# Kernel optimization log

Measured on AMD Instinct MI355X. Metric: run time of the kernel, lower is better.

## Reference

```python
import jax, jax.numpy as jnp
import numpy as np

N, S, EMB, H = 8, 1024, 512, 8
D = EMB // H  # head_dim = 64


def setup_inputs() -> dict:
    key = jax.random.key(0)
    ks = jax.random.split(key, 12)
    f = lambda k_, shp, s=1.0: jax.random.normal(k_, shp, dtype=jnp.float32) * s
    return {
        "v": f(ks[0], (N, S, EMB)),
        "k": f(ks[1], (N, S, EMB)),
        "q": f(ks[2], (N, S, EMB)),
        "Wv": f(ks[3], (D, D), 0.02), "bv": jnp.zeros((D,), jnp.float32),
        "Wk": f(ks[4], (D, D), 0.02), "bk": jnp.zeros((D,), jnp.float32),
        "Wq": f(ks[5], (D, D), 0.02), "bq": jnp.zeros((D,), jnp.float32),
        "E": f(ks[6], (1, S, D), 0.02),   # relative-position embedding
        "Wo": f(ks[7], (EMB, EMB), 0.02), "bo": jnp.zeros((EMB,), jnp.float32),
    }


def reference(v, k, q, Wv, bv, Wk, bk, Wq, bq, E, Wo, bo):
    n = v.shape[0]
    # per-head linear projections (module == 'spatiotemporal' branch)
    vals = v.reshape(n, S, H, D) @ Wv.T + bv   # (n,S,H,D)
    keys = k.reshape(n, S, H, D) @ Wk.T + bk
    qrs = q.reshape(n, S, H, D) @ Wq.T + bq

    # relative-position bias via skew trick (uses VALUES, as in source)
    QE = jnp.einsum('nlhd,sd->nhls', vals, E[0])            # (n,H,S,S)
    flip_mask = jnp.flip(jnp.triu(jnp.ones((S, S), bool), 1), axis=1)
    QE = jnp.where(flip_mask, 0.0, QE)                      # _mask_positions
    padded = jnp.pad(QE, ((0, 0), (0, 0), (0, 0), (1, 0)))  # left-pad last dim
    Sbias = padded.reshape(n, H, S + 1, S)[:, :, 1:, :]     # _skew -> (n,H,S,S)

    # attention scores with the source's mask semantics:
    # masked_fill(mask == 0, -1e20) keeps entries where triu(...,1) == 1
    qk = jnp.einsum('nqhd,nkhd->nhqk', qrs, keys)           # (n,H,S,S)
    keep = jnp.triu(jnp.ones((S, S), bool), 1)
    qk = jnp.where(keep, qk, jnp.float32(-1e20))

    attn = jax.nn.softmax(qk / jnp.sqrt(jnp.float32(EMB)), axis=3) + Sbias

    z = jnp.einsum('nhql,nlhd->nqhd', attn, vals).reshape(n, S, EMB)
    return z @ Wo.T + bo
```

## Files before the change

### kernel.cpp

```cpp
#include <hip/hip_runtime.h>
#include <hip/hip_bf16.h>

#define SDIM 1024
#define HNUM 8
#define DDIM 64
#define EMBD 512
#define NBATCH 8

static constexpr float SCALE = 0.044194173824159216f;

typedef short bf16x8 __attribute__((ext_vector_type(8)));
typedef float f32x4 __attribute__((ext_vector_type(4)));

__device__ __forceinline__ ushort bf16_of(float f) {
    return __builtin_bit_cast(unsigned short, __float2bfloat16(f));
}
__device__ __forceinline__ float f32_of(ushort u) {
    return __bfloat162float(__builtin_bit_cast(__hip_bfloat16, u));
}

__device__ __forceinline__ bf16x8 lds8(const ushort* base, int row, int slot) {
    return *(const bf16x8*)(base + (row * 8 + (slot ^ (row & 7))) * 8);
}

#define MFMA(a, b, c) __builtin_amdgcn_mfma_f32_16x16x32_bf16(a, b, c, 0, 0, 0)

__global__ __launch_bounds__(256) void proj_mfma(
    const float* __restrict__ xv, const float* __restrict__ xk, const float* __restrict__ xq,
    const float* __restrict__ Wv, const float* __restrict__ bv,
    const float* __restrict__ Wk, const float* __restrict__ bk,
    const float* __restrict__ Wq, const float* __restrict__ bq,
    ushort* __restrict__ vals_bf, ushort* __restrict__ keys_bf, ushort* __restrict__ qrs_bf)
{
    __shared__ ushort a_s[256 * 64];
    __shared__ ushort w_s[64 * 64];

    const int blk = blockIdx.x;
    const int m = blk % 3;
    const int chunk = blk / 3;
    const int tok0 = chunk * 32;
    const int n = tok0 >> 10, s0 = tok0 & 1023;
    const int t = threadIdx.x;
    const int w = t >> 6, l = t & 63, lrow = l & 15, lgrp = l >> 4;

    const float* X = (m == 0) ? xv : (m == 1) ? xk : xq;
    const float* W = (m == 0) ? Wv : (m == 1) ? Wk : Wq;
    const float* B = (m == 0) ? bv : (m == 1) ? bk : bq;
    ushort* O = (m == 0) ? vals_bf : (m == 1) ? keys_bf : qrs_bf;

    #pragma unroll
    for (int i = 0; i < 16; ++i) {
        const int f4 = i * 256 + t;
        const int ls = f4 >> 7, c4 = f4 & 127;
        const int h = c4 >> 4, d4 = c4 & 15;
        const float4 v = ((const float4*)(X + (size_t)(tok0 + ls) * EMBD))[c4];
        ushort4 u;
        u.x = bf16_of(v.x); u.y = bf16_of(v.y); u.z = bf16_of(v.z); u.w = bf16_of(v.w);
        const int r = h * 32 + ls, slot = d4 >> 1;
        *(ushort4*)(a_s + (r * 8 + (slot ^ (r & 7))) * 8 + (d4 & 1) * 4) = u;
    }
    #pragma unroll
    for (int i = 0; i < 4; ++i) {
        const int f4 = i * 256 + t;
        const int r = f4 >> 4, d4 = f4 & 15;
        const float4 v = ((const float4*)W)[f4];
        ushort4 u;
        u.x = bf16_of(v.x); u.y = bf16_of(v.y); u.z = bf16_of(v.z); u.w = bf16_of(v.w);
        const int slot = d4 >> 1;
        *(ushort4*)(w_s + (r * 8 + (slot ^ (r & 7))) * 8 + (d4 & 1) * 4) = u;
    }
    __syncthreads();

    f32x4 acc[4][4];
    #pragma unroll
    for (int fr = 0; fr < 4; ++fr)
        #pragma unroll
        for (int fc = 0; fc < 4; ++fc) acc[fr][fc] = {0.f, 0.f, 0.f, 0.f};

    bf16x8 af[4][2];
    #pragma unroll
    for (int fr = 0; fr < 4; ++fr)
        #pragma unroll
        for (int kc = 0; kc < 2; ++kc)
            af[fr][kc] = lds8(a_s, w * 64 + fr * 16 + lrow, lgrp + kc * 4);

    #pragma unroll
    for (int fc = 0; fc < 4; ++fc)
        #pragma unroll
        for (int kc = 0; kc < 2; ++kc) {
            const bf16x8 bfr = lds8(w_s, fc * 16 + lrow, lgrp + kc * 4);
            #pragma unroll
            for (int fr = 0; fr < 4; ++fr)
                acc[fr][fc] = MFMA(af[fr][kc], bfr, acc[fr][fc]);
        }
    __syncthreads();

    float bias[4];
    #pragma unroll
    for (int fc = 0; fc < 4; ++fc) bias[fc] = B[fc * 16 + lrow];
    #pragma unroll
    for (int fr = 0; fr < 4; ++fr)
        #pragma unroll
        for (int fc = 0; fc < 4; ++fc)
            #pragma unroll
            for (int reg = 0; reg < 4; ++reg) {
                const int row = w * 64 + fr * 16 + lgrp * 4 + reg;
                const int col = fc * 16 + lrow;
                a_s[(row * 8 + ((col >> 3) ^ (row & 7))) * 8 + (col & 7)] =
                    bf16_of(acc[fr][fc][reg] + bias[fc]);
            }
    __syncthreads();

    #pragma unroll
    for (int i = 0; i < 8; ++i) {
        const int cc = i * 256 + t;
        const int r = cc >> 3, slot = cc & 7;
        const int h = r >> 5, ls = r & 31;
        const float4 v = *(const float4*)(a_s + (r * 8 + (slot ^ (r & 7))) * 8);
        *(float4*)(O + ((size_t)(n * HNUM + h) * SDIM + s0 + ls) * DDIM + slot * 8) = v;
    }
}

__global__ __launch_bounds__(256) void conv_e(const float* __restrict__ E, ushort* __restrict__ e_bf) {
    const int i = blockIdx.x * 256 + threadIdx.x;
    e_bf[i] = bf16_of(E[i]);
}
__global__ __launch_bounds__(256) void conv_wo(const float* __restrict__ Wo, ushort* __restrict__ wo_bf) {
    const int i = blockIdx.x * 256 + threadIdx.x;
    wo_bf[i] = bf16_of(Wo[i]);
}

__global__ __launch_bounds__(256) void transpose_vals(
    const ushort* __restrict__ vals_bf, ushort* __restrict__ valsT_bf)
{
    __shared__ ushort tile[64][72];
    const int blk = blockIdx.x;
    const int st = blk & 15, nh = blk >> 4;
    const int s0 = st * 64;
    const int t = threadIdx.x;
    const ushort* src = vals_bf + (nh * SDIM + s0) * DDIM;
    #pragma unroll
    for (int i = 0; i < 2; ++i) {
        const int c = t + i * 256;
        const int row = c >> 3, slot = c & 7;
        const float4 vv = ((const float4*)src)[c];
        *(float4*)&tile[row][slot * 8] = vv;
    }
    __syncthreads();
    const int d = t >> 2, si = (t & 3) * 16;
    union { ushort u[16]; float4 f[2]; } buf;
    #pragma unroll
    for (int u2 = 0; u2 < 16; ++u2) buf.u[u2] = tile[si + u2][d];
    float4* dst = (float4*)(valsT_bf + (nh * DDIM + d) * SDIM + s0 + si);
    dst[0] = buf.f[0];
    dst[1] = buf.f[1];
}

__global__ __launch_bounds__(512, 2) void attn_mfma(
    const ushort* __restrict__ vals_bf, const ushort* __restrict__ keys_bf,
    const ushort* __restrict__ qrs_bf, const ushort* __restrict__ valsT_bf,
    const ushort* __restrict__ e_bf, ushort* __restrict__ zh)
{
    __shared__ ushort k_s [64 * 64];
    __shared__ ushort vt_s[64 * 64];
    __shared__ ushort e_s [192 * 64];
    __shared__ ushort pe_s[128 * 64];
    __shared__ ushort pb_s[128 * 64];
    __shared__ float  vs_s[64];

    const int vid = blockIdx.x;
    const int blk = (vid & 7) * 64 + (vid >> 3);
    const int bt = blk & 7, h = (blk >> 3) & 7, n = blk >> 6;
    const int i0 = bt * 128;
    const int t = threadIdx.x;
    const int w = t >> 6, l = t & 63, lrow = l & 15, lgrp = l >> 4;
    const int s = w >> 2, q = w & 3;
    const int myit = 2 * bt + s;
    const int eoff = (1 - s) * 64;

    const ushort* Qb  = qrs_bf   + (n * HNUM + h) * (SDIM * DDIM);
    const ushort* Kb  = keys_bf  + (n * HNUM + h) * (SDIM * DDIM);
    const ushort* Vb  = vals_bf  + (n * HNUM + h) * (SDIM * DDIM);
    const ushort* VTb = valsT_bf + (n * HNUM + h) * (SDIM * DDIM);

    bf16x8 a_q[2], a_vi[2];
    {
        const int grow = i0 + w * 16 + lrow;
        #pragma unroll
        for (int kc = 0; kc < 2; ++kc) {
            a_q[kc]  = *(const bf16x8*)(Qb + grow * DDIM + kc * 32 + lgrp * 8);
            a_vi[kc] = *(const bf16x8*)(Vb + grow * DDIM + kc * 32 + lgrp * 8);
        }
    }
    if (t < 64) vs_s[t] = 0.f;

    f32x4 accn[4], accz[4];
    #pragma unroll
    for (int f = 0; f < 4; ++f) {
        accn[f] = {0.f, 0.f, 0.f, 0.f};
        accz[f] = {0.f, 0.f, 0.f, 0.f};
    }
    float den[4] = {0.f, 0.f, 0.f, 0.f};

    for (int jt = 0; jt < 16; ++jt) {
        const int j0 = jt * 64;
        const bool diag = (jt == myit);
        const bool needK = (jt >= 2 * bt);
        const bool needE = (jt <= 2 * bt + 1);
        __syncthreads();

        {
            const int row = t >> 3, slot = t & 7;
            const int sw = (row * 8 + (slot ^ (row & 7))) * 8;
            *(float4*)(vt_s + sw) = *(const float4*)(VTb + row * SDIM + j0 + slot * 8);
            if (needK)
                *(float4*)(k_s + sw) = *(const float4*)(Kb + (j0 + row) * DDIM + slot * 8);
        }
        if (needE) {
            const int ebU = SDIM - 128 - i0 + j0;
            #pragma unroll
            for (int i = 0; i < 3; ++i) {
                const int c = t + i * 512;
                const int row = c >> 3, slot = c & 7;
                const int g = ebU + row;
                float4 vv = make_float4(0.f, 0.f, 0.f, 0.f);
                if (g < SDIM) vv = *(const float4*)(e_bf + g * DDIM + slot * 8);
                *(float4*)(e_s + (row * 8 + (slot ^ (row & 7))) * 8) = vv;
            }
        }
        __syncthreads();

        if (bt == 7 && t < 64) {
            float sum = 0.f;
            #pragma unroll
            for (int slot = 0; slot < 8; ++slot) {
                const bf16x8 vv = lds8(vt_s, t, slot);
                #pragma unroll
                for (int u = 0; u < 8; ++u) sum += f32_of((ushort)vv[u]);
            }
            vs_s[t] += sum;
        }

        if (jt >= myit) {
            f32x4 sf[4];
            #pragma unroll
            for (int fc = 0; fc < 4; ++fc) sf[fc] = {0.f, 0.f, 0.f, 0.f};
            #pragma unroll
            for (int fc = 0; fc < 4; ++fc)
                if (!diag || fc >= q)
                    #pragma unroll
                    for (int kc = 0; kc < 2; ++kc)
                        sf[fc] = MFMA(a_q[kc], lds8(k_s, fc * 16 + lrow, lgrp + kc * 4), sf[fc]);
            #pragma unroll
            for (int fc = 0; fc < 4; ++fc) {
                #pragma unroll
                for (int r = 0; r < 4; ++r) {
                    const int rs = q * 16 + lgrp * 4 + r;
                    const int col = fc * 16 + lrow;
                    float e = 0.f;
                    if (!diag || col > rs) e = __expf(sf[fc][r] * SCALE);
                    den[r] += e;
                    const int prow = w * 16 + lgrp * 4 + r;
                    pe_s[(prow * 8 + ((col >> 3) ^ (prow & 7))) * 8 + (col & 7)] = bf16_of(e);
                }
            }
            bf16x8 ap[2];
            #pragma unroll
            for (int kc = 0; kc < 2; ++kc) ap[kc] = lds8(pe_s, w * 16 + lrow, lgrp + kc * 4);
            #pragma unroll
            for (int fc = 0; fc < 4; ++fc)
                #pragma unroll
                for (int kc = 0; kc < 2; ++kc)
                    accn[fc] = MFMA(ap[kc], lds8(vt_s, fc * 16 + lrow, lgrp + kc * 4), accn[fc]);
        }

        if (jt <= myit) {
            #pragma unroll
            for (int half = 0; half < 2; ++half) {
                f32x4 bd[4];
                #pragma unroll
                for (int fq = 0; fq < 4; ++fq) bd[fq] = {0.f, 0.f, 0.f, 0.f};
                #pragma unroll
                for (int fq = 0; fq < 4; ++fq) {
                    const int fc = half * 4 + fq;
                    const bool live = diag ? (fc <= 3 && fc + q >= 3)
                                           : (fc + q >= 3 && fc + q <= 7);
                    if (live)
                        #pragma unroll
                        for (int kc = 0; kc < 2; ++kc)
                            bd[fq] = MFMA(a_vi[kc], lds8(e_s, eoff + fc * 16 + lrow, lgrp + kc * 4), bd[fq]);
                }
                #pragma unroll
                for (int fq = 0; fq < 4; ++fq) {
                    const int fc = half * 4 + fq;
                    const bool touch = diag ? true : (fc + q >= 3 && fc + q <= 7);
                    if (touch) {
                        #pragma unroll
                        for (int r = 0; r < 4; ++r) {
                            const int rs = q * 16 + lgrp * 4 + r;
                            const int u = fc * 16 + lrow;
                            const int c = u - 63 + rs;
                            if (c >= 0 && c < 64) {
                                const float val = (diag && u > 63) ? 0.f : bd[fq][r];
                                const int prow = w * 16 + lgrp * 4 + r;
                                pb_s[(prow * 8 + ((c >> 3) ^ (prow & 7))) * 8 + (c & 7)] = bf16_of(val);
                            }
                        }
                    }
                }
            }
            bf16x8 ap[2];
            #pragma unroll
            for (int kc = 0; kc < 2; ++kc) ap[kc] = lds8(pb_s, w * 16 + lrow, lgrp + kc * 4);
            #pragma unroll
            for (int fc = 0; fc < 4; ++fc)
                #pragma unroll
                for (int kc = 0; kc < 2; ++kc)
                    accz[fc] = MFMA(ap[kc], lds8(vt_s, fc * 16 + lrow, lgrp + kc * 4), accz[fc]);
        }
    }

    __syncthreads();

    #pragma unroll
    for (int r = 0; r < 4; ++r) {
        float d = den[r];
        d += __shfl_xor(d, 1);
        d += __shfl_xor(d, 2);
        d += __shfl_xor(d, 4);
        d += __shfl_xor(d, 8);
        den[r] = d;
    }

    #pragma unroll
    for (int fc = 0; fc < 4; ++fc) {
        #pragma unroll
        for (int r = 0; r < 4; ++r) {
            const int grow = i0 + w * 16 + lgrp * 4 + r;
            const int col = fc * 16 + lrow;
            float o;
            if (grow == SDIM - 1)
                o = vs_s[col] * (1.0f / SDIM) + accz[fc][r];
            else
                o = accn[fc][r] / den[r] + accz[fc][r];
            zh[(size_t)(n * SDIM + grow) * EMBD + h * DDIM + col] = bf16_of(o);
        }
    }
}

__global__ __launch_bounds__(256) void out_mfma(
    const ushort* __restrict__ zh, const ushort* __restrict__ wo_bf,
    const float* __restrict__ bo, float* __restrict__ out)
{
    __shared__ ushort ah_s[128 * 64];
    __shared__ ushort b_s [64 * 64];

    const int vid = blockIdx.x;
    const int blk = (vid & 7) * 64 + (vid >> 3);
    const int r0 = (blk >> 3) * 128, c0 = (blk & 7) * 64;
    const int t = threadIdx.x;
    const int w = t >> 6, l = t & 63, lrow = l & 15, lgrp = l >> 4;

    f32x4 acc[2][4];
    #pragma unroll
    for (int fr = 0; fr < 2; ++fr)
        #pragma unroll
        for (int fc = 0; fc < 4; ++fc) acc[fr][fc] = {0.f, 0.f, 0.f, 0.f};

    for (int kt = 0; kt < 8; ++kt) {
        __syncthreads();
        #pragma unroll
        for (int i = 0; i < 4; ++i) {
            const int cc = i * 256 + t;
            const int r = cc >> 3, slot = cc & 7;
            const size_t src = (size_t)(r0 + r) * EMBD + kt * 64 + slot * 8;
            *(float4*)(ah_s + (r * 8 + (slot ^ (r & 7))) * 8) = *(const float4*)(zh + src);
        }
        #pragma unroll
        for (int i = 0; i < 2; ++i) {
            const int cc = i * 256 + t;
            const int r = cc >> 3, slot = cc & 7;
            const float4 vb = *(const float4*)(wo_bf + (size_t)(c0 + r) * EMBD + kt * 64 + slot * 8);
            *(float4*)(b_s + (r * 8 + (slot ^ (r & 7))) * 8) = vb;
        }
        __syncthreads();

        #pragma unroll
        for (int kc = 0; kc < 2; ++kc)
            #pragma unroll
            for (int fc = 0; fc < 4; ++fc) {
                const bf16x8 bfr = lds8(b_s, fc * 16 + lrow, lgrp + kc * 4);
                #pragma unroll
                for (int fr = 0; fr < 2; ++fr)
                    acc[fr][fc] = MFMA(lds8(ah_s, w * 32 + fr * 16 + lrow, lgrp + kc * 4), bfr, acc[fr][fc]);
            }
    }

    float bias[4];
    #pragma unroll
    for (int fc = 0; fc < 4; ++fc) bias[fc] = bo[c0 + fc * 16 + lrow];
    #pragma unroll
    for (int fr = 0; fr < 2; ++fr)
        #pragma unroll
        for (int fc = 0; fc < 4; ++fc)
            #pragma unroll
            for (int reg = 0; reg < 4; ++reg) {
                const int row = r0 + w * 32 + fr * 16 + lgrp * 4 + reg;
                const int col = c0 + fc * 16 + lrow;
                out[(size_t)row * EMBD + col] = acc[fr][fc][reg] + bias[fc];
            }
}

extern "C" void kernel_launch(void* const* d_in, const int* in_sizes, int n_in,
                              void* d_out, int out_size, void* d_ws, size_t ws_size,
                              hipStream_t stream) {
    const float* v  = (const float*)d_in[0];
    const float* k  = (const float*)d_in[1];
    const float* q  = (const float*)d_in[2];
    const float* Wv = (const float*)d_in[3];
    const float* bv = (const float*)d_in[4];
    const float* Wk = (const float*)d_in[5];
    const float* bk = (const float*)d_in[6];
    const float* Wq = (const float*)d_in[7];
    const float* bq = (const float*)d_in[8];
    const float* E  = (const float*)d_in[9];
    const float* Wo = (const float*)d_in[10];
    const float* bo = (const float*)d_in[11];
    float* out = (float*)d_out;

    char* ws = (char*)d_ws;
    ushort* qrs_bf   = (ushort*)(ws);
    ushort* keys_bf  = (ushort*)(ws + ((size_t)8 << 20));
    ushort* vals_bf  = (ushort*)(ws + ((size_t)16 << 20));
    ushort* valsT_bf = (ushort*)(ws + ((size_t)24 << 20));
    ushort* e_bf     = (ushort*)(ws + ((size_t)32 << 20));
    ushort* wo_bf    = (ushort*)(ws + ((size_t)33 << 20));
    ushort* zh       = (ushort*)(ws + ((size_t)34 << 20));

    proj_mfma<<<768, 256, 0, stream>>>(v, k, q, Wv, bv, Wk, bk, Wq, bq,
                                       vals_bf, keys_bf, qrs_bf);
    conv_e<<<(SDIM * DDIM) / 256, 256, 0, stream>>>(E, e_bf);
    conv_wo<<<(EMBD * EMBD) / 256, 256, 0, stream>>>(Wo, wo_bf);
    transpose_vals<<<NBATCH * HNUM * 16, 256, 0, stream>>>(vals_bf, valsT_bf);
    attn_mfma<<<512, 512, 0, stream>>>(vals_bf, keys_bf, qrs_bf,
                                       valsT_bf, e_bf, zh);
    out_mfma<<<512, 256, 0, stream>>>(zh, wo_bf, bo, out);
}
```

Before: 116.2 us.

## Restructure attention kernel into 64-row blocks with register operands and double-buffered K

The attention kernel now uses 256-thread blocks, each covering 64 query rows, and launches twice as many blocks. V^T and E fragments load straight from global memory into registers instead of being staged in LDS, and Q and V fragments are reloaded each iteration rather than held. Only K is staged, through a double-buffered LDS tile with one barrier per iteration, and the score and bias tiles share one LDS buffer. The aim is less LDS use and fewer barriers, which raises occupancy; the cost is more global/L2 traffic for the V^T and E fragments. It also adds s_setprio around MFMA sections and computes the last-row value sum with shuffles.

```diff
diff --git a/kernel.cpp b/kernel.cpp
--- a/kernel.cpp
+++ b/kernel.cpp
@@ -156,43 +156,27 @@
     dst[1] = buf.f[1];
 }
 
-__global__ __launch_bounds__(512, 2) void attn_mfma(
+__global__ __launch_bounds__(256, 4) void attn_mfma(
     const ushort* __restrict__ vals_bf, const ushort* __restrict__ keys_bf,
     const ushort* __restrict__ qrs_bf, const ushort* __restrict__ valsT_bf,
     const ushort* __restrict__ e_bf, ushort* __restrict__ zh)
 {
-    __shared__ ushort k_s [64 * 64];
-    __shared__ ushort vt_s[64 * 64];
-    __shared__ ushort e_s [192 * 64];
-    __shared__ ushort pe_s[128 * 64];
-    __shared__ ushort pb_s[128 * 64];
-    __shared__ float  vs_s[64];
+    __shared__ ushort kbuf[2][64 * 64];
+    __shared__ ushort p_s[64 * 64];
 
     const int vid = blockIdx.x;
-    const int blk = (vid & 7) * 64 + (vid >> 3);
-    const int bt = blk & 7, h = (blk >> 3) & 7, n = blk >> 6;
-    const int i0 = bt * 128;
+    const int blk = (vid & 7) * 128 + (vid >> 3);
+    const int it = blk & 15, h = (blk >> 4) & 7, n = blk >> 7;
+    const int i0 = it * 64;
     const int t = threadIdx.x;
     const int w = t >> 6, l = t & 63, lrow = l & 15, lgrp = l >> 4;
-    const int s = w >> 2, q = w & 3;
-    const int myit = 2 * bt + s;
-    const int eoff = (1 - s) * 64;
 
     const ushort* Qb  = qrs_bf   + (n * HNUM + h) * (SDIM * DDIM);
     const ushort* Kb  = keys_bf  + (n * HNUM + h) * (SDIM * DDIM);
     const ushort* Vb  = vals_bf  + (n * HNUM + h) * (SDIM * DDIM);
     const ushort* VTb = valsT_bf + (n * HNUM + h) * (SDIM * DDIM);
 
-    bf16x8 a_q[2], a_vi[2];
-    {
-        const int grow = i0 + w * 16 + lrow;
-        #pragma unroll
-        for (int kc = 0; kc < 2; ++kc) {
-            a_q[kc]  = *(const bf16x8*)(Qb + grow * DDIM + kc * 32 + lgrp * 8);
-            a_vi[kc] = *(const bf16x8*)(Vb + grow * DDIM + kc * 32 + lgrp * 8);
-        }
-    }
-    if (t < 64) vs_s[t] = 0.f;
+    const int grow0 = i0 + w * 16 + lrow;
 
     f32x4 accn[4], accz[4];
     #pragma unroll
@@ -201,80 +185,43 @@
         accz[f] = {0.f, 0.f, 0.f, 0.f};
     }
     float den[4] = {0.f, 0.f, 0.f, 0.f};
+    float vsum[4] = {0.f, 0.f, 0.f, 0.f};
+
+    const int sr0 = t >> 3, sr1 = (t >> 3) + 32, ss = t & 7;
+
+    {
+        const float4 k0 = *(const float4*)(Kb + (it * 64 + sr0) * DDIM + ss * 8);
+        const float4 k1 = *(const float4*)(Kb + (it * 64 + sr1) * DDIM + ss * 8);
+        ushort* kb = kbuf[it & 1];
+        *(float4*)(kb + (sr0 * 8 + (ss ^ (sr0 & 7))) * 8) = k0;
+        *(float4*)(kb + (sr1 * 8 + (ss ^ (sr1 & 7))) * 8) = k1;
+    }
+    __syncthreads();
 
     for (int jt = 0; jt < 16; ++jt) {
         const int j0 = jt * 64;
-        const bool diag = (jt == myit);
-        const bool needK = (jt >= 2 * bt);
-        const bool needE = (jt <= 2 * bt + 1);
-        __syncthreads();
-
-        {
-            const int row = t >> 3, slot = t & 7;
-            const int sw = (row * 8 + (slot ^ (row & 7))) * 8;
-            *(float4*)(vt_s + sw) = *(const float4*)(VTb + row * SDIM + j0 + slot * 8);
-            if (needK)
-                *(float4*)(k_s + sw) = *(const float4*)(Kb + (j0 + row) * DDIM + slot * 8);
-        }
-        if (needE) {
-            const int ebU = SDIM - 128 - i0 + j0;
-            #pragma unroll
-            for (int i = 0; i < 3; ++i) {
-                const int c = t + i * 512;
-                const int row = c >> 3, slot = c & 7;
-                const int g = ebU + row;
-                float4 vv = make_float4(0.f, 0.f, 0.f, 0.f);
-                if (g < SDIM) vv = *(const float4*)(e_bf + g * DDIM + slot * 8);
-                *(float4*)(e_s + (row * 8 + (slot ^ (row & 7))) * 8) = vv;
-            }
-        }
-        __syncthreads();
-
-        if (bt == 7 && t < 64) {
-            float sum = 0.f;
-            #pragma unroll
-            for (int slot = 0; slot < 8; ++slot) {
-                const bf16x8 vv = lds8(vt_s, t, slot);
-                #pragma unroll
-                for (int u = 0; u < 8; ++u) sum += f32_of((ushort)vv[u]);
-            }
-            vs_s[t] += sum;
-        }
-
-        if (jt >= myit) {
-            f32x4 sf[4];
-            #pragma unroll
-            for (int fc = 0; fc < 4; ++fc) sf[fc] = {0.f, 0.f, 0.f, 0.f};
-            #pragma unroll
-            for (int fc = 0; fc < 4; ++fc)
-                if (!diag || fc >= q)
-                    #pragma unroll
-                    for (int kc = 0; kc < 2; ++kc)
-                        sf[fc] = MFMA(a_q[kc], lds8(k_s, fc * 16 + lrow, lgrp + kc * 4), sf[fc]);
-            #pragma unroll
-            for (int fc = 0; fc < 4; ++fc) {
-                #pragma unroll
-                for (int r = 0; r < 4; ++r) {
-                    const int rs = q * 16 + lgrp * 4 + r;
-                    const int col = fc * 16 + lrow;
-                    float e = 0.f;
-                    if (!diag || col > rs) e = __expf(sf[fc][r] * SCALE);
-                    den[r] += e;
-                    const int prow = w * 16 + lgrp * 4 + r;
-                    pe_s[(prow * 8 + ((col >> 3) ^ (prow & 7))) * 8 + (col & 7)] = bf16_of(e);
-                }
-            }
-            bf16x8 ap[2];
-            #pragma unroll
-            for (int kc = 0; kc < 2; ++kc) ap[kc] = lds8(pe_s, w * 16 + lrow, lgrp + kc * 4);
-            #pragma unroll
-            for (int fc = 0; fc < 4; ++fc)
-                #pragma unroll
-                for (int kc = 0; kc < 2; ++kc)
-                    accn[fc] = MFMA(ap[kc], lds8(vt_s, fc * 16 + lrow, lgrp + kc * 4), accn[fc]);
-        }
-
-        if (jt <= myit) {
+        const bool diag = (jt == it);
+        const bool stg = (jt >= it) && (jt < 15);
+
+        bf16x8 vtf[4][2];
+        #pragma unroll
+        for (int fc = 0; fc < 4; ++fc)
+            #pragma unroll
+            for (int kc = 0; kc < 2; ++kc)
+                vtf[fc][kc] = *(const bf16x8*)(VTb + (fc * 16 + lrow) * SDIM + j0 + kc * 32 + lgrp * 8);
+
+        float4 k0, k1;
+        if (stg) {
+            k0 = *(const float4*)(Kb + ((jt + 1) * 64 + sr0) * DDIM + ss * 8);
+            k1 = *(const float4*)(Kb + ((jt + 1) * 64 + sr1) * DDIM + ss * 8);
+        }
+
+        if (jt <= it) {
+            bf16x8 a_vi[2];
+            #pragma unroll
+            for (int kc = 0; kc < 2; ++kc)
+                a_vi[kc] = *(const bf16x8*)(Vb + grow0 * DDIM + kc * 32 + lgrp * 8);
+            const int eb = SDIM - 64 - i0 + j0;
             #pragma unroll
             for (int half = 0; half < 2; ++half) {
                 f32x4 bd[4];
@@ -283,44 +230,102 @@
                 #pragma unroll
                 for (int fq = 0; fq < 4; ++fq) {
                     const int fc = half * 4 + fq;
-                    const bool live = diag ? (fc <= 3 && fc + q >= 3)
-                                           : (fc + q >= 3 && fc + q <= 7);
-                    if (live)
+                    if (fc + w >= 3 && fc + w <= 7) {
+                        const int g = eb + fc * 16 + lrow;
                         #pragma unroll
-                        for (int kc = 0; kc < 2; ++kc)
-                            bd[fq] = MFMA(a_vi[kc], lds8(e_s, eoff + fc * 16 + lrow, lgrp + kc * 4), bd[fq]);
+                        for (int kc = 0; kc < 2; ++kc) {
+                            bf16x8 ef = {0, 0, 0, 0, 0, 0, 0, 0};
+                            if (g < SDIM)
+                                ef = *(const bf16x8*)(e_bf + g * DDIM + kc * 32 + lgrp * 8);
+                            bd[fq] = MFMA(a_vi[kc], ef, bd[fq]);
+                        }
+                    }
                 }
                 #pragma unroll
                 for (int fq = 0; fq < 4; ++fq) {
                     const int fc = half * 4 + fq;
-                    const bool touch = diag ? true : (fc + q >= 3 && fc + q <= 7);
-                    if (touch) {
+                    if (fc + w >= 3 && fc + w <= 7) {
+                        const int u = fc * 16 + lrow;
                         #pragma unroll
                         for (int r = 0; r < 4; ++r) {
-                            const int rs = q * 16 + lgrp * 4 + r;
-                            const int u = fc * 16 + lrow;
+                            const int rs = w * 16 + lgrp * 4 + r;
                             const int c = u - 63 + rs;
-                            if (c >= 0 && c < 64) {
-                                const float val = (diag && u > 63) ? 0.f : bd[fq][r];
-                                const int prow = w * 16 + lgrp * 4 + r;
-                                pb_s[(prow * 8 + ((c >> 3) ^ (prow & 7))) * 8 + (c & 7)] = bf16_of(val);
-                            }
+                            if (c >= 0 && c < 64)
+                                p_s[(rs * 8 + ((c >> 3) ^ (rs & 7))) * 8 + (c & 7)] = bf16_of(bd[fq][r]);
                         }
                     }
                 }
             }
             bf16x8 ap[2];
             #pragma unroll
-            for (int kc = 0; kc < 2; ++kc) ap[kc] = lds8(pb_s, w * 16 + lrow, lgrp + kc * 4);
+            for (int kc = 0; kc < 2; ++kc) ap[kc] = lds8(p_s, w * 16 + lrow, lgrp + kc * 4);
+            __builtin_amdgcn_s_setprio(1);
             #pragma unroll
             for (int fc = 0; fc < 4; ++fc)
                 #pragma unroll
                 for (int kc = 0; kc < 2; ++kc)
-                    accz[fc] = MFMA(ap[kc], lds8(vt_s, fc * 16 + lrow, lgrp + kc * 4), accz[fc]);
-        }
-    }
-
-    __syncthreads();
+                    accz[fc] = MFMA(ap[kc], vtf[fc][kc], accz[fc]);
+            __builtin_amdgcn_s_setprio(0);
+        }
+
+        if (jt >= it) {
+            const ushort* kb = kbuf[jt & 1];
+            bf16x8 aq[2];
+            #pragma unroll
+            for (int kc = 0; kc < 2; ++kc)
+                aq[kc] = *(const bf16x8*)(Qb + grow0 * DDIM + kc * 32 + lgrp * 8);
+            f32x4 sf[4];
+            #pragma unroll
+            for (int fc = 0; fc < 4; ++fc) sf[fc] = {0.f, 0.f, 0.f, 0.f};
+            __builtin_amdgcn_s_setprio(1);
+            #pragma unroll
+            for (int fc = 0; fc < 4; ++fc)
+                if (!diag || fc >= w)
+                    #pragma unroll
+                    for (int kc = 0; kc < 2; ++kc)
+                        sf[fc] = MFMA(aq[kc], lds8(kb, fc * 16 + lrow, lgrp + kc * 4), sf[fc]);
+            __builtin_amdgcn_s_setprio(0);
+            #pragma unroll
+            for (int fc = 0; fc < 4; ++fc) {
+                #pragma unroll
+                for (int r = 0; r < 4; ++r) {
+                    const int rs = w * 16 + lgrp * 4 + r;
+                    const int col = fc * 16 + lrow;
+                    float e = 0.f;
+                    if (!diag || col > rs) e = __expf(sf[fc][r] * SCALE);
+                    den[r] += e;
+                    p_s[(rs * 8 + ((col >> 3) ^ (rs & 7))) * 8 + (col & 7)] = bf16_of(e);
+                }
+            }
+            bf16x8 ap[2];
+            #pragma unroll
+            for (int kc = 0; kc < 2; ++kc) ap[kc] = lds8(p_s, w * 16 + lrow, lgrp + kc * 4);
+            __builtin_amdgcn_s_setprio(1);
+            #pragma unroll
+            for (int fc = 0; fc < 4; ++fc)
+                #pragma unroll
+                for (int kc = 0; kc < 2; ++kc)
+                    accn[fc] = MFMA(ap[kc], vtf[fc][kc], accn[fc]);
+            __builtin_amdgcn_s_setprio(0);
+        }
+
+        if (it == 15 && w == 3) {
+            #pragma unroll
+            for (int fc = 0; fc < 4; ++fc)
+                #pragma unroll
+                for (int kc = 0; kc < 2; ++kc)
+                    #pragma unroll
+                    for (int u = 0; u < 8; ++u)
+                        vsum[fc] += f32_of((ushort)vtf[fc][kc][u]);
+        }
+
+        if (stg) {
+            ushort* kb = kbuf[(jt + 1) & 1];
+            *(float4*)(kb + (sr0 * 8 + (ss ^ (sr0 & 7))) * 8) = k0;
+            *(float4*)(kb + (sr1 * 8 + (ss ^ (sr1 & 7))) * 8) = k1;
+            __syncthreads();
+        }
+    }
 
     #pragma unroll
     for (int r = 0; r < 4; ++r) {
@@ -331,6 +336,14 @@
         d += __shfl_xor(d, 8);
         den[r] = d;
     }
+    float vsr[4];
+    #pragma unroll
+    for (int fc = 0; fc < 4; ++fc) {
+        float vv = vsum[fc];
+        vv += __shfl_xor(vv, 16);
+        vv += __shfl_xor(vv, 32);
+        vsr[fc] = vv;
+    }
 
     #pragma unroll
     for (int fc = 0; fc < 4; ++fc) {
@@ -340,7 +353,7 @@
             const int col = fc * 16 + lrow;
             float o;
             if (grow == SDIM - 1)
-                o = vs_s[col] * (1.0f / SDIM) + accz[fc][r];
+                o = vsr[fc] * (1.0f / SDIM) + accz[fc][r];
             else
                 o = accn[fc][r] / den[r] + accz[fc][r];
             zh[(size_t)(n * SDIM + grow) * EMBD + h * DDIM + col] = bf16_of(o);
@@ -442,7 +455,7 @@
     conv_e<<<(SDIM * DDIM) / 256, 256, 0, stream>>>(E, e_bf);
     conv_wo<<<(EMBD * EMBD) / 256, 256, 0, stream>>>(Wo, wo_bf);
     transpose_vals<<<NBATCH * HNUM * 16, 256, 0, stream>>>(vals_bf, valsT_bf);
-    attn_mfma<<<512, 512, 0, stream>>>(vals_bf, keys_bf, qrs_bf,
-                                       valsT_bf, e_bf, zh);
+    attn_mfma<<<NBATCH * HNUM * 16, 256, 0, stream>>>(vals_bf, keys_bf, qrs_bf,
+                                                      valsT_bf, e_bf, zh);
     out_mfma<<<512, 256, 0, stream>>>(zh, wo_bf, bo, out);
 }
```

Result: slower. 259.2 us (+123.0%).
